# Kernel optimization log

Measured on AMD Instinct MI355X. Metric: run time of the kernel, lower is better.

## Reference

```python
import jax, jax.numpy as jnp
import numpy as np


def setup_inputs() -> dict:
    key = jax.random.key(0)
    ks = jax.random.split(key, 5)
    B, C_in, C_out, E, H, W = 32, 256, 256, 8, 56, 56
    Ch = C_in // 4
    x = jax.random.normal(ks[0], (B, C_in, H, W), dtype=jnp.float32)
    # expert kernel bank, stored [E, C_out, C_in] (1x1 kernels)
    weights = jax.random.normal(ks[1], (E, C_out, C_in), dtype=jnp.float32) * (1.0 / np.sqrt(C_in))
    # attention generator: 1x1 convs == linear layers on pooled features
    w1 = jax.random.normal(ks[2], (Ch, C_in), dtype=jnp.float32) * (1.0 / np.sqrt(C_in))
    b1 = jnp.zeros((Ch,), dtype=jnp.float32)
    w2 = jax.random.normal(ks[3], (E, Ch), dtype=jnp.float32) * (1.0 / np.sqrt(Ch))
    b2 = jnp.zeros((E,), dtype=jnp.float32)
    return {"x": x, "weights": weights, "w1": w1, "b1": b1, "w2": w2, "b2": b2}


def reference(x, weights, w1, b1, w2, b2):
    # x: [B, C_in, H, W]; weights: [E, C_out, C_in]
    # attn_generator: global avg pool -> 1x1 conv -> relu -> 1x1 conv
    pooled = jnp.mean(x, axis=(2, 3))                      # [B, C_in]
    h = jax.nn.relu(pooled @ w1.T + b1)                    # [B, C_in//4]
    logits = h @ w2.T + b2                                 # [B, E]
    attn = jax.nn.softmax(logits, axis=1)                  # softmax over experts
    # per-sample fused 1x1 kernel: sum_e attn[b,e] * weights[e]
    w_dyn = jnp.einsum('be,eoc->boc', attn, weights)       # [B, C_out, C_in]
    # grouped 1x1 conv with groups=B == per-sample matmul over channels
    out = jnp.einsum('boc,bchw->bohw', w_dyn, x)           # [B, C_out, H, W]
    return out
```

## Files before the change

kernel.cpp:

```cpp
#include <hip/hip_runtime.h>
#include <hip/hip_bf16.h>

typedef unsigned short u16;
typedef __attribute__((ext_vector_type(8))) short short8;
typedef __attribute__((ext_vector_type(4))) float floatx4;

__device__ __forceinline__ u16 f32_to_bf16_rne(float f) {
  union { float f; unsigned int u; } v; v.f = f;
  unsigned int u = v.u;
  u += 0x7FFFu + ((u >> 16) & 1u);
  return (u16)(u >> 16);
}

__device__ __forceinline__ void load_lds_16(const void* gsrc, void* lds) {
  __builtin_amdgcn_global_load_lds(
      (const __attribute__((address_space(1))) unsigned int*)gsrc,
      (__attribute__((address_space(3))) unsigned int*)lds,
      16, 0, 0);
}

__global__ __launch_bounds__(256) void pool_kernel(const float* __restrict__ x,
                                                   float* __restrict__ pooled) {
  const int bc = blockIdx.x;
  const float4* row = (const float4*)(x + (size_t)bc * 3136);
  const int t = threadIdx.x;
  float s = 0.0f;
  for (int q = t; q < 784; q += 256) {
    float4 v = row[q];
    s += (v.x + v.y) + (v.z + v.w);
  }
  #pragma unroll
  for (int off = 32; off > 0; off >>= 1) s += __shfl_down(s, off, 64);
  __shared__ float red[4];
  if ((t & 63) == 0) red[t >> 6] = s;
  __syncthreads();
  if (t == 0) pooled[bc] = (red[0] + red[1] + red[2] + red[3]) * (1.0f / 3136.0f);
}

__global__ __launch_bounds__(256) void attn_wdyn_kernel(
    const float* __restrict__ pooled, const float* __restrict__ weights,
    const float* __restrict__ w1, const float* __restrict__ b1,
    const float* __restrict__ w2, const float* __restrict__ b2,
    u16* __restrict__ wdyn) {
  const int blk = blockIdx.x;
  const int b = blk >> 3;
  const int oc = blk & 7;
  const int t = threadIdx.x;
  __shared__ float ph[256];
  __shared__ float part[256];
  __shared__ float hb[64];
  __shared__ float lg[8];
  ph[t] = pooled[b * 256 + t];
  __syncthreads();
  {
    const int row = t >> 2, seg = t & 3;
    const float* wr = w1 + row * 256 + seg * 64;
    const float* pp = ph + seg * 64;
    float a = 0.0f;
    #pragma unroll 8
    for (int c = 0; c < 64; ++c) a += pp[c] * wr[c];
    part[t] = a;
  }
  __syncthreads();
  if (t < 64) {
    float a = part[t * 4] + part[t * 4 + 1] + part[t * 4 + 2] + part[t * 4 + 3] + b1[t];
    hb[t] = fmaxf(a, 0.0f);
  }
  __syncthreads();
  if (t < 64) {
    const int row = t >> 3, seg = t & 7;
    const float* wr = w2 + row * 64 + seg * 8;
    float a = 0.0f;
    #pragma unroll
    for (int j = 0; j < 8; ++j) a += hb[seg * 8 + j] * wr[j];
    part[t] = a;
  }
  __syncthreads();
  if (t < 8) {
    float a = b2[t];
    #pragma unroll
    for (int j = 0; j < 8; ++j) a += part[t * 8 + j];
    lg[t] = a;
  }
  __syncthreads();
  float a[8];
  {
    float mx = lg[0];
    #pragma unroll
    for (int e = 1; e < 8; ++e) mx = fmaxf(mx, lg[e]);
    float sum = 0.0f;
    #pragma unroll
    for (int e = 0; e < 8; ++e) { a[e] = __expf(lg[e] - mx); sum += a[e]; }
    float inv = 1.0f / sum;
    #pragma unroll
    for (int e = 0; e < 8; ++e) a[e] *= inv;
  }
  const int o0 = oc * 32;
  for (int i = 0; i < 32; ++i) {
    const int o = o0 + i;
    float acc = 0.0f;
    #pragma unroll
    for (int e = 0; e < 8; ++e)
      acc += a[e] * weights[((size_t)e * 256 + o) * 256 + t];
    wdyn[((size_t)b * 256 + o) * 256 + t] = f32_to_bf16_rne(acc);
  }
}

#define BM 256
#define BN 64
#define BK 32
#define XP 40

__global__ __launch_bounds__(256) void dynconv_gemm(const float* __restrict__ x,
                                                    const u16* __restrict__ wdyn,
                                                    float* __restrict__ out) {
  const int nb = blockIdx.x;
  const int b  = blockIdx.y;
  const int t = threadIdx.x;
  const int lane = t & 63;
  const int wv = t >> 6;
  const int quad = lane >> 4;
  const int l16 = lane & 15;

  __shared__ u16 Ws[BM * BK];
  __shared__ u16 Xs[BN * XP];

  const float* xb = x + (size_t)b * (256 * 3136);
  const u16* wb = wdyn + (size_t)b * 256 * 256;
  float* ob = out + (size_t)b * 256 * 3136;
  const int n0 = nb * BN;

  floatx4 acc[4][4];
  #pragma unroll
  for (int i = 0; i < 4; ++i)
    #pragma unroll
    for (int j = 0; j < 4; ++j) acc[i][j] = (floatx4)(0.0f);

  const int xn = lane;
  const int xkg = wv;

  for (int kt = 0; kt < 8; ++kt) {
    const int k0 = kt * BK;
    #pragma unroll
    for (int j = 0; j < 4; ++j) {
      const int i = j * 256 + t;
      const int r = i >> 2;
      const int c8 = i & 3;
      load_lds_16(wb + r * 256 + k0 + c8 * 8, &Ws[i * 8]);
    }
    {
      const float* xs = xb + (size_t)(k0 + xkg * 8) * 3136 + n0 + xn;
      float v[8];
      #pragma unroll
      for (int j = 0; j < 8; ++j) v[j] = xs[(size_t)j * 3136];
      short8 pk;
      #pragma unroll
      for (int j = 0; j < 4; ++j) {
        __hip_bfloat162 h2 = __float22bfloat162_rn(make_float2(v[2 * j], v[2 * j + 1]));
        union { __hip_bfloat162 h; struct { short lo, hi; } s; } u; u.h = h2;
        pk[2 * j] = u.s.lo; pk[2 * j + 1] = u.s.hi;
      }
      *(short8*)(&Xs[xn * XP + xkg * 8]) = pk;
    }
    __syncthreads();
    short8 bfr[4];
    #pragma unroll
    for (int nt = 0; nt < 4; ++nt) {
      const int n = nt * 16 + l16;
      bfr[nt] = *(const short8*)(&Xs[n * XP + quad * 8]);
    }
    #pragma unroll
    for (int mt = 0; mt < 4; ++mt) {
      const int r = wv * 64 + mt * 16 + l16;
      short8 af = *(const short8*)(&Ws[r * BK + quad * 8]);
      #pragma unroll
      for (int nt = 0; nt < 4; ++nt)
        acc[mt][nt] = __builtin_amdgcn_mfma_f32_16x16x32_bf16(
            af, bfr[nt], acc[mt][nt], 0, 0, 0);
    }
    __syncthreads();
  }
  #pragma unroll
  for (int mt = 0; mt < 4; ++mt) {
    const int orow = wv * 64 + mt * 16 + quad * 4;
    #pragma unroll
    for (int nt = 0; nt < 4; ++nt) {
      const int n = n0 + nt * 16 + l16;
      #pragma unroll
      for (int r = 0; r < 4; ++r)
        ob[(size_t)(orow + r) * 3136 + n] = acc[mt][nt][r];
    }
  }
}

extern "C" void kernel_launch(void* const* d_in, const int* in_sizes, int n_in,
                              void* d_out, int out_size, void* d_ws, size_t ws_size,
                              hipStream_t stream) {
  const float* x       = (const float*)d_in[0];
  const float* weights = (const float*)d_in[1];
  const float* w1      = (const float*)d_in[2];
  const float* b1      = (const float*)d_in[3];
  const float* w2      = (const float*)d_in[4];
  const float* b2      = (const float*)d_in[5];
  float* out = (float*)d_out;

  float* pooled = (float*)d_ws;
  u16* wdyn = (u16*)((char*)d_ws + 32768);

  pool_kernel<<<8192, 256, 0, stream>>>(x, pooled);
  attn_wdyn_kernel<<<256, 256, 0, stream>>>(pooled, weights, w1, b1, w2, b2, wdyn);
  dynconv_gemm<<<dim3(49, 32), 256, 0, stream>>>(x, wdyn, out);
}
```

Before: 231.7 us.

## Fuse pooling with bf16 transpose of x and double-buffer the GEMM

```diff
diff --git a/kernel.cpp b/kernel.cpp
--- a/kernel.cpp
+++ b/kernel.cpp
@@ -2,8 +2,10 @@
 #include <hip/hip_bf16.h>
 
 typedef unsigned short u16;
+typedef unsigned int u32;
 typedef __attribute__((ext_vector_type(8))) short short8;
 typedef __attribute__((ext_vector_type(4))) float floatx4;
+typedef __attribute__((ext_vector_type(4))) u32 uint4v;
 
 __device__ __forceinline__ u16 f32_to_bf16_rne(float f) {
   union { float f; unsigned int u; } v; v.f = f;
@@ -18,6 +20,216 @@
       (__attribute__((address_space(3))) unsigned int*)lds,
       16, 0, 0);
 }
+
+
+__global__ __launch_bounds__(256) void transpose_pool_kernel(
+    const float* __restrict__ x, u16* __restrict__ xT, float* __restrict__ pp) {
+  const int nb = blockIdx.x;
+  const int b  = blockIdx.y;
+  const int t  = threadIdx.x;
+  const int l  = t & 15;
+  const int r  = t >> 4;
+  const int n0 = nb * 64;
+
+  __shared__ __align__(16) u16 T[64][66];
+  __shared__ float poolacc[256];
+
+  const float* xb = x + (size_t)b * (256 * 3136);
+  u16* xTb = xT + ((size_t)b * 3136 + n0) * 256;
+
+  for (int cc = 0; cc < 4; ++cc) {
+    #pragma unroll
+    for (int j = 0; j < 4; ++j) {
+      const int c_local = j * 16 + r;
+      const int c = cc * 64 + c_local;
+      float4 v = *(const float4*)(xb + (size_t)c * 3136 + n0 + l * 4);
+      float s = (v.x + v.y) + (v.z + v.w);
+      s += __shfl_down(s, 8, 16);
+      s += __shfl_down(s, 4, 16);
+      s += __shfl_down(s, 2, 16);
+      s += __shfl_down(s, 1, 16);
+      if (l == 0) poolacc[c] = s;
+      T[l * 4 + 0][c_local] = f32_to_bf16_rne(v.x);
+      T[l * 4 + 1][c_local] = f32_to_bf16_rne(v.y);
+      T[l * 4 + 2][c_local] = f32_to_bf16_rne(v.z);
+      T[l * 4 + 3][c_local] = f32_to_bf16_rne(v.w);
+    }
+    __syncthreads();
+    {
+      const int nl = t >> 2;
+      const int s4 = t & 3;
+      u32 dw[8];
+      #pragma unroll
+      for (int u = 0; u < 8; ++u)
+        dw[u] = *(const u32*)&T[nl][s4 * 16 + u * 2];
+      u16* dst = xTb + (size_t)nl * 256 + cc * 64 + s4 * 16;
+      *(uint4v*)dst       = (uint4v){dw[0], dw[1], dw[2], dw[3]};
+      *(uint4v*)(dst + 8) = (uint4v){dw[4], dw[5], dw[6], dw[7]};
+    }
+    __syncthreads();
+  }
+  pp[((size_t)b * 49 + nb) * 256 + t] = poolacc[t];
+}
+
+__global__ __launch_bounds__(256) void attn_wdyn_kernel2(
+    const float* __restrict__ pp, const float* __restrict__ weights,
+    const float* __restrict__ w1, const float* __restrict__ b1,
+    const float* __restrict__ w2, const float* __restrict__ b2,
+    u16* __restrict__ wdyn) {
+  const int blk = blockIdx.x;
+  const int b = blk >> 3;
+  const int oc = blk & 7;
+  const int t = threadIdx.x;
+  __shared__ float ph[256];
+  __shared__ float part[256];
+  __shared__ float hb[64];
+  __shared__ float lg[8];
+  {
+    float s = 0.0f;
+    const float* pb = pp + (size_t)b * 49 * 256 + t;
+    #pragma unroll 7
+    for (int j = 0; j < 49; ++j) s += pb[j * 256];
+    ph[t] = s * (1.0f / 3136.0f);
+  }
+  __syncthreads();
+  {
+    const int row = t >> 2, seg = t & 3;
+    const float* wr = w1 + row * 256 + seg * 64;
+    const float* ppx = ph + seg * 64;
+    float a = 0.0f;
+    #pragma unroll 8
+    for (int c = 0; c < 64; ++c) a += ppx[c] * wr[c];
+    part[t] = a;
+  }
+  __syncthreads();
+  if (t < 64) {
+    float a = part[t * 4] + part[t * 4 + 1] + part[t * 4 + 2] + part[t * 4 + 3] + b1[t];
+    hb[t] = fmaxf(a, 0.0f);
+  }
+  __syncthreads();
+  if (t < 64) {
+    const int row = t >> 3, seg = t & 7;
+    const float* wr = w2 + row * 64 + seg * 8;
+    float a = 0.0f;
+    #pragma unroll
+    for (int j = 0; j < 8; ++j) a += hb[seg * 8 + j] * wr[j];
+    part[t] = a;
+  }
+  __syncthreads();
+  if (t < 8) {
+    float a = b2[t];
+    #pragma unroll
+    for (int j = 0; j < 8; ++j) a += part[t * 8 + j];
+    lg[t] = a;
+  }
+  __syncthreads();
+  float a[8];
+  {
+    float mx = lg[0];
+    #pragma unroll
+    for (int e = 1; e < 8; ++e) mx = fmaxf(mx, lg[e]);
+    float sum = 0.0f;
+    #pragma unroll
+    for (int e = 0; e < 8; ++e) { a[e] = __expf(lg[e] - mx); sum += a[e]; }
+    float inv = 1.0f / sum;
+    #pragma unroll
+    for (int e = 0; e < 8; ++e) a[e] *= inv;
+  }
+  const int o0 = oc * 32;
+  for (int i = 0; i < 32; ++i) {
+    const int o = o0 + i;
+    float acc = 0.0f;
+    #pragma unroll
+    for (int e = 0; e < 8; ++e)
+      acc += a[e] * weights[((size_t)e * 256 + o) * 256 + t];
+    wdyn[((size_t)b * 256 + o) * 256 + t] = f32_to_bf16_rne(acc);
+  }
+}
+
+#define BM 256
+#define BN 64
+#define BK 32
+#define XP 40
+
+__global__ __launch_bounds__(256) void dynconv_gemm2(
+    const u16* __restrict__ xT, const u16* __restrict__ wdyn,
+    float* __restrict__ out) {
+  const int nb = blockIdx.x;
+  const int b  = blockIdx.y;
+  const int t = threadIdx.x;
+  const int lane = t & 63;
+  const int wv = t >> 6;
+  const int quad = lane >> 4;
+  const int l16 = lane & 15;
+  const int n0 = nb * BN;
+
+  __shared__ __align__(16) u16 Ws[2][BM * BK];
+  __shared__ __align__(16) u16 Xs[2][BN * BK];
+
+  const u16* wb = wdyn + (size_t)b * 256 * 256;
+  const u16* xn = xT + ((size_t)b * 3136 + n0) * 256;
+  float* ob = out + (size_t)b * 256 * 3136 + n0;
+
+  const int wq = (t & 3) ^ ((t >> 3) & 3);
+  const int rw = t >> 2;
+
+  floatx4 acc[4][4];
+  #pragma unroll
+  for (int i = 0; i < 4; ++i)
+    #pragma unroll
+    for (int j = 0; j < 4; ++j) acc[i][j] = (floatx4)(0.0f);
+
+  #define STAGE(bf, kt)                                                        \
+    do {                                                                       \
+      const int k0_ = (kt) * BK;                                               \
+      _Pragma("unroll")                                                        \
+      for (int j = 0; j < 4; ++j) {                                            \
+        const int rr_ = j * 64 + rw;                                           \
+        load_lds_16(wb + (size_t)rr_ * 256 + k0_ + wq * 8,                     \
+                    &Ws[bf][(j * 256 + t) * 8]);                               \
+      }                                                                        \
+      load_lds_16(xn + (size_t)rw * 256 + k0_ + wq * 8, &Xs[bf][t * 8]);       \
+    } while (0)
+
+  STAGE(0, 0);
+  __syncthreads();
+
+  const int qs = (quad ^ ((l16 >> 1) & 3)) * 8;
+
+  int cur = 0;
+  for (int kt = 0; kt < 8; ++kt) {
+    if (kt < 7) STAGE(cur ^ 1, kt + 1);
+    short8 bfr[4];
+    #pragma unroll
+    for (int nt = 0; nt < 4; ++nt)
+      bfr[nt] = *(const short8*)&Xs[cur][(nt * 16 + l16) * BK + qs];
+    #pragma unroll
+    for (int mt = 0; mt < 4; ++mt) {
+      const int rr = wv * 64 + mt * 16 + l16;
+      short8 af = *(const short8*)&Ws[cur][rr * BK + qs];
+      #pragma unroll
+      for (int nt = 0; nt < 4; ++nt)
+        acc[mt][nt] = __builtin_amdgcn_mfma_f32_16x16x32_bf16(
+            af, bfr[nt], acc[mt][nt], 0, 0, 0);
+    }
+    __syncthreads();
+    cur ^= 1;
+  }
+  #undef STAGE
+
+  #pragma unroll
+  for (int mt = 0; mt < 4; ++mt) {
+    const int orow = wv * 64 + mt * 16 + quad * 4;
+    #pragma unroll
+    for (int nt = 0; nt < 4; ++nt) {
+      const int n = nt * 16 + l16;
+      #pragma unroll
+      for (int rg = 0; rg < 4; ++rg)
+        ob[(size_t)(orow + rg) * 3136 + n] = acc[mt][nt][rg];
+    }
+  }
+}
+
 
 __global__ __launch_bounds__(256) void pool_kernel(const float* __restrict__ x,
                                                    float* __restrict__ pooled) {
@@ -106,11 +318,6 @@
   }
 }
 
-#define BM 256
-#define BN 64
-#define BK 32
-#define XP 40
-
 __global__ __launch_bounds__(256) void dynconv_gemm(const float* __restrict__ x,
                                                     const u16* __restrict__ wdyn,
                                                     float* __restrict__ out) {
@@ -122,8 +329,8 @@
   const int quad = lane >> 4;
   const int l16 = lane & 15;
 
-  __shared__ u16 Ws[BM * BK];
-  __shared__ u16 Xs[BN * XP];
+  __shared__ u16 Wf[BM * BK];
+  __shared__ u16 Xf[BN * XP];
 
   const float* xb = x + (size_t)b * (256 * 3136);
   const u16* wb = wdyn + (size_t)b * 256 * 256;
@@ -136,7 +343,7 @@
     #pragma unroll
     for (int j = 0; j < 4; ++j) acc[i][j] = (floatx4)(0.0f);
 
-  const int xn = lane;
+  const int xnn = lane;
   const int xkg = wv;
 
   for (int kt = 0; kt < 8; ++kt) {
@@ -146,10 +353,10 @@
       const int i = j * 256 + t;
       const int r = i >> 2;
       const int c8 = i & 3;
-      load_lds_16(wb + r * 256 + k0 + c8 * 8, &Ws[i * 8]);
+      load_lds_16(wb + r * 256 + k0 + c8 * 8, &Wf[i * 8]);
     }
     {
-      const float* xs = xb + (size_t)(k0 + xkg * 8) * 3136 + n0 + xn;
+      const float* xs = xb + (size_t)(k0 + xkg * 8) * 3136 + n0 + xnn;
       float v[8];
       #pragma unroll
       for (int j = 0; j < 8; ++j) v[j] = xs[(size_t)j * 3136];
@@ -160,19 +367,19 @@
         union { __hip_bfloat162 h; struct { short lo, hi; } s; } u; u.h = h2;
         pk[2 * j] = u.s.lo; pk[2 * j + 1] = u.s.hi;
       }
-      *(short8*)(&Xs[xn * XP + xkg * 8]) = pk;
+      *(short8*)(&Xf[xnn * XP + xkg * 8]) = pk;
     }
     __syncthreads();
     short8 bfr[4];
     #pragma unroll
     for (int nt = 0; nt < 4; ++nt) {
       const int n = nt * 16 + l16;
-      bfr[nt] = *(const short8*)(&Xs[n * XP + quad * 8]);
+      bfr[nt] = *(const short8*)(&Xf[n * XP + quad * 8]);
     }
     #pragma unroll
     for (int mt = 0; mt < 4; ++mt) {
       const int r = wv * 64 + mt * 16 + l16;
-      short8 af = *(const short8*)(&Ws[r * BK + quad * 8]);
+      short8 af = *(const short8*)(&Wf[r * BK + quad * 8]);
       #pragma unroll
       for (int nt = 0; nt < 4; ++nt)
         acc[mt][nt] = __builtin_amdgcn_mfma_f32_16x16x32_bf16(
@@ -192,6 +399,7 @@
     }
   }
 }
+
 
 extern "C" void kernel_launch(void* const* d_in, const int* in_sizes, int n_in,
                               void* d_out, int out_size, void* d_ws, size_t ws_size,
@@ -204,10 +412,25 @@
   const float* b2      = (const float*)d_in[5];
   float* out = (float*)d_out;
 
-  float* pooled = (float*)d_ws;
-  u16* wdyn = (u16*)((char*)d_ws + 32768);
-
-  pool_kernel<<<8192, 256, 0, stream>>>(x, pooled);
-  attn_wdyn_kernel<<<256, 256, 0, stream>>>(pooled, weights, w1, b1, w2, b2, wdyn);
-  dynconv_gemm<<<dim3(49, 32), 256, 0, stream>>>(x, wdyn, out);
-}
+  const size_t PP_SZ    = (size_t)32 * 49 * 256 * 4;
+  const size_t WDYN_OFF = PP_SZ;
+  const size_t WDYN_SZ  = (size_t)32 * 256 * 256 * 2;
+  const size_t XT_OFF   = WDYN_OFF + WDYN_SZ;
+  const size_t XT_SZ    = (size_t)32 * 3136 * 256 * 2;
+  const size_t NEED     = XT_OFF + XT_SZ;
+
+  if (ws_size >= NEED) {
+    float* pp = (float*)d_ws;
+    u16* wdyn = (u16*)((char*)d_ws + WDYN_OFF);
+    u16* xT   = (u16*)((char*)d_ws + XT_OFF);
+    transpose_pool_kernel<<<dim3(49, 32), 256, 0, stream>>>(x, xT, pp);
+    attn_wdyn_kernel2<<<256, 256, 0, stream>>>(pp, weights, w1, b1, w2, b2, wdyn);
+    dynconv_gemm2<<<dim3(49, 32), 256, 0, stream>>>(xT, wdyn, out);
+  } else {
+    float* pooled = (float*)d_ws;
+    u16* wdyn = (u16*)((char*)d_ws + 32768);
+    pool_kernel<<<8192, 256, 0, stream>>>(x, pooled);
+    attn_wdyn_kernel<<<256, 256, 0, stream>>>(pooled, weights, w1, b1, w2, b2, wdyn);
+    dynconv_gemm<<<dim3(49, 32), 256, 0, stream>>>(x, wdyn, out);
+  }
+}
```

Result: slower. 244.5 us (+5.5%).

## Double-buffer X tile, load W fragments directly to registers, swizzle LDS

Applied to the files above, without the earlier changes.

```diff
diff --git a/kernel.cpp b/kernel.cpp
--- a/kernel.cpp
+++ b/kernel.cpp
@@ -10,13 +10,6 @@
   unsigned int u = v.u;
   u += 0x7FFFu + ((u >> 16) & 1u);
   return (u16)(u >> 16);
-}
-
-__device__ __forceinline__ void load_lds_16(const void* gsrc, void* lds) {
-  __builtin_amdgcn_global_load_lds(
-      (const __attribute__((address_space(1))) unsigned int*)gsrc,
-      (__attribute__((address_space(3))) unsigned int*)lds,
-      16, 0, 0);
 }
 
 __global__ __launch_bounds__(256) void pool_kernel(const float* __restrict__ x,
@@ -106,14 +99,11 @@
   }
 }
 
-#define BM 256
-#define BN 64
 #define BK 32
-#define XP 40
-
-__global__ __launch_bounds__(256) void dynconv_gemm(const float* __restrict__ x,
-                                                    const u16* __restrict__ wdyn,
-                                                    float* __restrict__ out) {
+
+__global__ __launch_bounds__(256) void dynconv_gemm3(
+    const float* __restrict__ x, const u16* __restrict__ wdyn,
+    float* __restrict__ out) {
   const int nb = blockIdx.x;
   const int b  = blockIdx.y;
   const int t = threadIdx.x;
@@ -121,14 +111,18 @@
   const int wv = t >> 6;
   const int quad = lane >> 4;
   const int l16 = lane & 15;
-
-  __shared__ u16 Ws[BM * BK];
-  __shared__ u16 Xs[BN * XP];
-
-  const float* xb = x + (size_t)b * (256 * 3136);
-  const u16* wb = wdyn + (size_t)b * 256 * 256;
-  float* ob = out + (size_t)b * 256 * 3136;
-  const int n0 = nb * BN;
+  const int n0 = nb * 64;
+
+  __shared__ __align__(16) u16 Xs[2][64 * BK];
+
+  const float* xb = x + (size_t)b * (256 * 3136) + n0 + lane;
+  const u16* wb = wdyn + (size_t)b * 65536;
+  float* ob = out + (size_t)b * (256 * 3136) + n0;
+
+  const u16* wfp = wb + (size_t)(wv * 64 + l16) * 256 + quad * 8;
+
+  const int wchunk = (wv ^ ((lane >> 1) & 3)) * 8;
+  const int rchunk = (quad ^ ((l16 >> 1) & 3)) * 8;
 
   floatx4 acc[4][4];
   #pragma unroll
@@ -136,59 +130,72 @@
     #pragma unroll
     for (int j = 0; j < 4; ++j) acc[i][j] = (floatx4)(0.0f);
 
-  const int xn = lane;
-  const int xkg = wv;
-
+  short8 wcur[4];
+  #pragma unroll
+  for (int mt = 0; mt < 4; ++mt)
+    wcur[mt] = *(const short8*)(wfp + mt * 16 * 256);
+  {
+    float xr[8];
+    #pragma unroll
+    for (int j = 0; j < 8; ++j) xr[j] = xb[(size_t)(wv * 8 + j) * 3136];
+    short8 pk;
+    #pragma unroll
+    for (int j = 0; j < 4; ++j) {
+      __hip_bfloat162 h2 = __float22bfloat162_rn(make_float2(xr[2 * j], xr[2 * j + 1]));
+      union { __hip_bfloat162 h; struct { short lo, hi; } s; } u; u.h = h2;
+      pk[2 * j] = u.s.lo; pk[2 * j + 1] = u.s.hi;
+    }
+    *(short8*)(&Xs[0][lane * BK + wchunk]) = pk;
+  }
+  __syncthreads();
+
+  int cur = 0;
   for (int kt = 0; kt < 8; ++kt) {
-    const int k0 = kt * BK;
-    #pragma unroll
-    for (int j = 0; j < 4; ++j) {
-      const int i = j * 256 + t;
-      const int r = i >> 2;
-      const int c8 = i & 3;
-      load_lds_16(wb + r * 256 + k0 + c8 * 8, &Ws[i * 8]);
-    }
-    {
-      const float* xs = xb + (size_t)(k0 + xkg * 8) * 3136 + n0 + xn;
-      float v[8];
-      #pragma unroll
-      for (int j = 0; j < 8; ++j) v[j] = xs[(size_t)j * 3136];
+    short8 wnxt[4];
+    float xr[8];
+    if (kt < 7) {
+      const int k1 = (kt + 1) * BK;
+      #pragma unroll
+      for (int j = 0; j < 8; ++j) xr[j] = xb[(size_t)(k1 + wv * 8 + j) * 3136];
+      #pragma unroll
+      for (int mt = 0; mt < 4; ++mt)
+        wnxt[mt] = *(const short8*)(wfp + mt * 16 * 256 + k1);
+    }
+    short8 bfr[4];
+    #pragma unroll
+    for (int nt = 0; nt < 4; ++nt)
+      bfr[nt] = *(const short8*)(&Xs[cur][(nt * 16 + l16) * BK + rchunk]);
+    #pragma unroll
+    for (int mt = 0; mt < 4; ++mt)
+      #pragma unroll
+      for (int nt = 0; nt < 4; ++nt)
+        acc[mt][nt] = __builtin_amdgcn_mfma_f32_16x16x32_bf16(
+            wcur[mt], bfr[nt], acc[mt][nt], 0, 0, 0);
+    if (kt < 7) {
       short8 pk;
       #pragma unroll
       for (int j = 0; j < 4; ++j) {
-        __hip_bfloat162 h2 = __float22bfloat162_rn(make_float2(v[2 * j], v[2 * j + 1]));
+        __hip_bfloat162 h2 = __float22bfloat162_rn(make_float2(xr[2 * j], xr[2 * j + 1]));
         union { __hip_bfloat162 h; struct { short lo, hi; } s; } u; u.h = h2;
         pk[2 * j] = u.s.lo; pk[2 * j + 1] = u.s.hi;
       }
-      *(short8*)(&Xs[xn * XP + xkg * 8]) = pk;
+      *(short8*)(&Xs[cur ^ 1][lane * BK + wchunk]) = pk;
+      #pragma unroll
+      for (int mt = 0; mt < 4; ++mt) wcur[mt] = wnxt[mt];
     }
     __syncthreads();
-    short8 bfr[4];
+    cur ^= 1;
+  }
+
+  #pragma unroll
+  for (int mt = 0; mt < 4; ++mt) {
+    const int orow = wv * 64 + mt * 16 + quad * 4;
     #pragma unroll
     for (int nt = 0; nt < 4; ++nt) {
       const int n = nt * 16 + l16;
-      bfr[nt] = *(const short8*)(&Xs[n * XP + quad * 8]);
-    }
-    #pragma unroll
-    for (int mt = 0; mt < 4; ++mt) {
-      const int r = wv * 64 + mt * 16 + l16;
-      short8 af = *(const short8*)(&Ws[r * BK + quad * 8]);
-      #pragma unroll
-      for (int nt = 0; nt < 4; ++nt)
-        acc[mt][nt] = __builtin_amdgcn_mfma_f32_16x16x32_bf16(
-            af, bfr[nt], acc[mt][nt], 0, 0, 0);
-    }
-    __syncthreads();
-  }
-  #pragma unroll
-  for (int mt = 0; mt < 4; ++mt) {
-    const int orow = wv * 64 + mt * 16 + quad * 4;
-    #pragma unroll
-    for (int nt = 0; nt < 4; ++nt) {
-      const int n = n0 + nt * 16 + l16;
-      #pragma unroll
-      for (int r = 0; r < 4; ++r)
-        ob[(size_t)(orow + r) * 3136 + n] = acc[mt][nt][r];
+      #pragma unroll
+      for (int rg = 0; rg < 4; ++rg)
+        ob[(size_t)(orow + rg) * 3136 + n] = acc[mt][nt][rg];
     }
   }
 }
@@ -209,5 +216,5 @@
 
   pool_kernel<<<8192, 256, 0, stream>>>(x, pooled);
   attn_wdyn_kernel<<<256, 256, 0, stream>>>(pooled, weights, w1, b1, w2, b2, wdyn);
-  dynconv_gemm<<<dim3(49, 32), 256, 0, stream>>>(x, wdyn, out);
-}
+  dynconv_gemm3<<<dim3(49, 32), 256, 0, stream>>>(x, wdyn, out);
+}
```

Result: no change. 235.7 us (+1.7%).
